# Kernel optimization log

Measured on AMD Instinct MI355X. Metric: run time of the kernel, lower is better.

Reference implementation:

```python
import jax, jax.numpy as jnp
import numpy as np

B, H, W, E = 8, 64, 64, 256  # channels == embedding (required by final Multiply)


def setup_inputs() -> dict:
    key = jax.random.key(0)
    k1, k2, k3 = jax.random.split(key, 3)
    inputs = jax.random.normal(k1, (B, H, W, E), dtype=jnp.float32)
    # Conv2D(embedding, 3, padding='same') params, HWIO layout
    conv_w = jax.random.normal(k2, (3, 3, E, E), dtype=jnp.float32) * (1.0 / np.sqrt(9 * E))
    conv_b = jnp.zeros((E,), dtype=jnp.float32)
    return {"inputs": inputs, "conv_w": conv_w, "conv_b": conv_b}


def reference(inputs, conv_w, conv_b):
    emb = conv_w.shape[-1]
    # conv1: 3x3 same-padded conv, NHWC
    x = jax.lax.conv_general_dilated(
        inputs, conv_w, window_strides=(1, 1), padding="SAME",
        dimension_numbers=("NHWC", "HWIO", "NHWC")) + conv_b
    b, h, w, e = x.shape
    x1 = x.reshape(b, h * w, e)                       # [B, N, E]
    scores = jnp.einsum("bne,bme->bnm", x1, x1)       # [B, N, N]
    attn = jax.nn.softmax(scores, axis=-1) / jnp.sqrt(jnp.asarray(emb, x.dtype))
    out = jnp.einsum("bnm,bme->bne", attn, x1)        # [B, N, E]
    # Original keras uses Reshape((inputs.shape[-2], inputs.shape[-3], -1)): (W, H, E)
    out = out.reshape(b, w, h, e)
    return out * inputs
```

## Files before the change

### kernel.cpp

```cpp
#include <hip/hip_runtime.h>
#include <hip/hip_bf16.h>

typedef __attribute__((ext_vector_type(4))) float f32x4;
typedef __attribute__((ext_vector_type(8))) _Float16 f16x8;
typedef __attribute__((ext_vector_type(16))) float f32x16;
typedef unsigned short u16;

#define NB 8
#define NE 256
#define NN 4096
#define SD 64

__device__ __forceinline__ f32x16 z16() {
  f32x16 v;
#pragma unroll
  for (int i = 0; i < 16; ++i) v[i] = 0.f;
  return v;
}
__device__ __forceinline__ void gload_lds16(const void* g, void* l) {
  __builtin_amdgcn_global_load_lds((const __attribute__((address_space(1))) void*)g,
                                   (__attribute__((address_space(3))) void*)l, 16, 0, 0);
}
__device__ __forceinline__ float fexp2(float x) {
#if __has_builtin(__builtin_amdgcn_exp2f)
  return __builtin_amdgcn_exp2f(x);
#else
  return exp2f(x);
#endif
}

#if __has_builtin(__builtin_amdgcn_permlane32_swap)
typedef int i32x2 __attribute__((ext_vector_type(2)));
__device__ __forceinline__ void plswap(int& a, int& b) {
  i32x2 r = __builtin_amdgcn_permlane32_swap(a, b, false, false);
  a = r[0]; b = r[1];
}
#else
__device__ __forceinline__ void plswap(int& a, int& b) {
  int xa = __shfl_xor(a, 32), xb = __shfl_xor(b, 32);
  int hi = (int)((threadIdx.x & 63) >> 5);
  int na = hi ? xb : a;
  int nb = hi ? b : xa;
  a = na; b = nb;
}
#endif

__global__ __launch_bounds__(256) void k_split(const float* __restrict__ x,
                                               u16* __restrict__ outF, int n4) {
  int i = blockIdx.x * 256 + threadIdx.x;
  if (i >= n4) return;
  float4 v = reinterpret_cast<const float4*>(x)[i];
  ushort4 o;
  o.x = __builtin_bit_cast(u16, (_Float16)v.x);
  o.y = __builtin_bit_cast(u16, (_Float16)v.y);
  o.z = __builtin_bit_cast(u16, (_Float16)v.z);
  o.w = __builtin_bit_cast(u16, (_Float16)v.w);
  reinterpret_cast<ushort4*>(outF)[i] = o;
}

__global__ __launch_bounds__(256) void k_wsplit(const float* __restrict__ w,
                                                u16* __restrict__ wT) {
  int i = blockIdx.x * 256 + threadIdx.x;
  int t = i >> 16;
  int r = i & 65535;
  int ei = r >> 8, eo = r & 255;
  int o = (t << 16) + (eo << 8) + ei;
  wT[o] = __builtin_bit_cast(u16, (_Float16)w[i]);
}

__global__ __launch_bounds__(256, 2) void k_conv(const u16* __restrict__ inF,
                                                 const u16* __restrict__ wT,
                                                 const float* __restrict__ bias,
                                                 u16* __restrict__ x1h) {
  __shared__ u16 Ah[128][72];
  __shared__ u16 BhL[128 * 64];
  int b = blockIdx.x >> 6;
  int rem = blockIdx.x & 63;
  int mt = rem >> 1, et = rem & 1;
  int h0 = mt << 1;
  int tid = threadIdx.x;
  int wid = tid >> 6, lane = tid & 63;
  int wr = wid >> 1, wc = wid & 1;
  int r = lane & 15, g = lane >> 4;
  f32x4 acc[4][4];
#pragma unroll
  for (int i = 0; i < 4; ++i)
#pragma unroll
    for (int j = 0; j < 4; ++j) acc[i][j] = (f32x4){0.f, 0.f, 0.f, 0.f};
  const long ibase = (long)b * NN * NE;
  const int bsw = ((((lane & 7) << 4) ^ (((lane >> 3) & 7) << 4)) >> 1);

#pragma unroll 1
  for (int t = 0; t < 9; ++t) {
    int dy = t / 3 - 1, dx = t % 3 - 1;
#pragma unroll 1
    for (int kc = 0; kc < 4; ++kc) {
      __syncthreads();
      for (int c = tid; c < 1024; c += 256) {
        int pix = c >> 3, c8 = c & 7;
        int ww = pix & 63, hh = h0 + (pix >> 6);
        int sh = hh + dy, sw = ww + dx;
        float4 vh = make_float4(0.f, 0.f, 0.f, 0.f);
        if ((unsigned)sh < 64u && (unsigned)sw < 64u) {
          long off = ibase + ((long)sh * 64 + sw) * NE + kc * 64 + c8 * 8;
          vh = *reinterpret_cast<const float4*>(inF + off);
        }
        *reinterpret_cast<float4*>(&Ah[pix][c8 * 8]) = vh;
      }
#pragma unroll
      for (int i = 0; i < 4; ++i) {
        int c = wid * 4 + i;
        int eo = c * 8 + (lane >> 3);
        const u16* src = wT + ((long)t << 16) + (long)(et * 128 + eo) * 256 + kc * 64 + bsw;
        gload_lds16(src, (char*)BhL + c * 1024);
      }
      __syncthreads();
#pragma unroll
      for (int ks = 0; ks < 2; ++ks) {
        int c8 = ks * 4 + g;
        f16x8 ah[4], bh[4];
#pragma unroll
        for (int mi = 0; mi < 4; ++mi)
          ah[mi] = *reinterpret_cast<const f16x8*>(&Ah[wr * 64 + mi * 16 + r][c8 * 8]);
#pragma unroll
        for (int ni = 0; ni < 4; ++ni) {
          int col = wc * 64 + ni * 16 + r;
          int byteoff = (col << 7) + (((c8 << 4) ^ ((r & 7) << 4)));
          bh[ni] = *reinterpret_cast<const f16x8*>(reinterpret_cast<const char*>(BhL) + byteoff);
        }
#pragma unroll
        for (int mi = 0; mi < 4; ++mi)
#pragma unroll
          for (int ni = 0; ni < 4; ++ni)
            acc[mi][ni] = __builtin_amdgcn_mfma_f32_16x16x32_f16(ah[mi], bh[ni], acc[mi][ni], 0, 0, 0);
      }
    }
  }
#pragma unroll
  for (int mi = 0; mi < 4; ++mi)
#pragma unroll
    for (int ni = 0; ni < 4; ++ni) {
      int eo = et * 128 + wc * 64 + ni * 16 + r;
      float bz = bias[eo];
#pragma unroll
      for (int i = 0; i < 4; ++i) {
        int pix = mt * 128 + wr * 64 + mi * 16 + g * 4 + i;
        float v = acc[mi][ni][i] + bz;
        long o = ibase + (long)pix * NE + eo;
        x1h[o] = __builtin_bit_cast(u16, (_Float16)v);
      }
    }
}

__global__ __launch_bounds__(256) void k_trans(const u16* __restrict__ x1h, u16* __restrict__ x1T) {
  __shared__ u16 T[64][72];
  int bid = blockIdx.x;
  int b = bid >> 8, rem = bid & 255;
  int mt = rem >> 2, et = rem & 3;
  int tid = threadIdx.x;
  for (int c = tid; c < 512; c += 256) {
    int rr = c >> 3, c8 = c & 7;
    *reinterpret_cast<float4*>(&T[rr][c8 * 8]) =
        *reinterpret_cast<const float4*>(x1h + ((long)b * NN + mt * 64 + rr) * NE + et * 64 + c8 * 8);
  }
  __syncthreads();
  for (int c = tid; c < 512; c += 256) {
    int er = c >> 3, m8 = c & 7;
    union { u16 u[8]; float4 v; } p;
#pragma unroll
    for (int j = 0; j < 8; ++j) p.u[j] = T[m8 * 8 + j][er];
    *reinterpret_cast<float4*>(x1T + ((long)b * NE + et * 64 + er) * NN + mt * 64 + m8 * 8) = p.v;
  }
}

__global__ __launch_bounds__(256, 2) void k_flash3(const u16* __restrict__ x1h16,
                                                   const u16* __restrict__ x1T,
                                                   const float* __restrict__ inp,
                                                   float* __restrict__ out) {
  __shared__ char LDS[65536];
  int phys = blockIdx.x;
  int b = phys & 7;
  int qt = phys >> 3;
  int tid = threadIdx.x, wid = tid >> 6, lane = tid & 63;
  int r31 = lane & 31, hi = lane >> 5;
  int eh = wid & 1, qg = wid >> 1;
  const long bN = (long)b << 12;
  const long vtb = (long)b << 20;

  const long qrow = bN + qt * 64 + qg * 32 + r31;
  f16x8 qh[16];
#pragma unroll
  for (int ks = 0; ks < 16; ++ks) {
    qh[ks] = *reinterpret_cast<const f16x8*>(x1h16 + (qrow << 8) + ks * 16 + hi * 8);
#pragma unroll
    for (int j = 0; j < 8; ++j)
      qh[ks][j] = (_Float16)((float)qh[ks][j] * 1.44269504f);
  }

  f32x16 o4[4];
#pragma unroll
  for (int nf = 0; nf < 4; ++nf) o4[nf] = z16();
  float mrow = -1.0e30f, lrow = 0.f;

  const u16* kS[4];
  const u16* vS[4];
  int off[4];
#pragma unroll
  for (int i = 0; i < 4; ++i) {
    int c = wid * 4 + i;
    off[i] = c << 10;
    int kr = c * 2 + (lane >> 5);
    int kcolb = ((lane & 31) << 4) ^ ((kr & 15) << 4);
    kS[i] = x1h16 + ((bN + kr) << 8) + (kcolb >> 1);
    int rp = c * 16 + (lane >> 2);
    int e = rp ^ ((rp >> 2) & 1);
    int vcolb = ((lane & 3) << 4) ^ ((e & 3) << 4);
    vS[i] = x1T + vtb + ((long)e << 12) + (vcolb >> 1);
  }

#pragma unroll
  for (int i = 0; i < 4; ++i) { gload_lds16(kS[i], LDS + off[i]); kS[i] += 8192; }
#pragma unroll
  for (int i = 0; i < 4; ++i) { gload_lds16(vS[i], LDS + 32768 + off[i]); vS[i] += 32; }

#pragma unroll 1
  for (int it = 0; it < 128; ++it) {
    const char* KB = LDS + (it & 1) * 16384;
    const char* VB = LDS + 32768 + (it & 1) * 16384;

    asm volatile("s_waitcnt vmcnt(0)" ::: "memory");
    __builtin_amdgcn_s_barrier();
    __builtin_amdgcn_sched_barrier(0);

    if (it < 127) {
      char* KD = LDS + ((it + 1) & 1) * 16384;
      char* VD = LDS + 32768 + ((it + 1) & 1) * 16384;
#pragma unroll
      for (int i = 0; i < 4; ++i) { gload_lds16(kS[i], KD + off[i]); kS[i] += 8192; }
#pragma unroll
      for (int i = 0; i < 4; ++i) { gload_lds16(vS[i], VD + off[i]); vS[i] += 32; }
    }

    f32x16 stA = z16(), stB = z16();
    int swzk = (r31 & 15) << 4;
    int krow = r31 << 9;
    __builtin_amdgcn_s_setprio(1);
#pragma unroll
    for (int ks = 0; ks < 8; ++ks) {
      int cbyA = ((2 * ks) * 32 + hi * 16) ^ swzk;
      int cbyB = ((2 * ks + 1) * 32 + hi * 16) ^ swzk;
      f16x8 kA = *reinterpret_cast<const f16x8*>(KB + krow + cbyA);
      f16x8 kB = *reinterpret_cast<const f16x8*>(KB + krow + cbyB);
      stA = __builtin_amdgcn_mfma_f32_32x32x16_f16(kA, qh[2 * ks], stA, 0, 0, 0);
      stB = __builtin_amdgcn_mfma_f32_32x32x16_f16(kB, qh[2 * ks + 1], stB, 0, 0, 0);
    }
    __builtin_amdgcn_s_setprio(0);
    f32x16 st;
#pragma unroll
    for (int m = 0; m < 16; ++m) st[m] = stA[m] + stB[m];

    float t8[8];
#pragma unroll
    for (int m = 0; m < 8; ++m) t8[m] = fmaxf(st[m], st[m + 8]);
    float t4a = fmaxf(t8[0], t8[4]), t4b = fmaxf(t8[1], t8[5]);
    float t4c = fmaxf(t8[2], t8[6]), t4d = fmaxf(t8[3], t8[7]);
    float tmax = fmaxf(fmaxf(t4a, t4b), fmaxf(t4c, t4d));
    tmax = fmaxf(tmax, __shfl_xor(tmax, 32));
    if (!__all(tmax <= mrow + 11.54f)) {
      float mnew = fmaxf(mrow, tmax);
      float alpha = fexp2(mrow - mnew);
      lrow *= alpha;
      float ar[16];
#pragma unroll
      for (int m = 0; m < 16; ++m) ar[m] = __shfl(alpha, (m & 3) + 8 * (m >> 2) + 4 * hi);
#pragma unroll
      for (int nf = 0; nf < 4; ++nf)
#pragma unroll
        for (int m = 0; m < 16; ++m) o4[nf][m] *= ar[m];
      mrow = mnew;
    }
#pragma unroll
    for (int m = 0; m < 16; ++m) st[m] = fexp2(st[m] - mrow);
    float s8[8];
#pragma unroll
    for (int m = 0; m < 8; ++m) s8[m] = st[m] + st[m + 8];
    float s4a = s8[0] + s8[4], s4b = s8[1] + s8[5], s4c = s8[2] + s8[6], s4d = s8[3] + s8[7];
    float psum = (s4a + s4b) + (s4c + s4d);
    psum += __shfl_xor(psum, 32);
    lrow += psum;

    int Wd[8];
#pragma unroll
    for (int m = 0; m < 8; ++m) {
      unsigned l0 = __builtin_bit_cast(u16, (_Float16)st[2 * m]);
      unsigned h0 = __builtin_bit_cast(u16, (_Float16)st[2 * m + 1]);
      Wd[m] = (int)(l0 | (h0 << 16));
    }
    plswap(Wd[0], Wd[2]); plswap(Wd[1], Wd[3]);
    plswap(Wd[4], Wd[6]); plswap(Wd[5], Wd[7]);
    union PU { int w[4]; f16x8 v; };
    PU pa[2];
#pragma unroll
    for (int c = 0; c < 2; ++c) {
      pa[c].w[0] = Wd[c * 4 + 0]; pa[c].w[1] = Wd[c * 4 + 1];
      pa[c].w[2] = Wd[c * 4 + 2]; pa[c].w[3] = Wd[c * 4 + 3];
    }

    __builtin_amdgcn_s_setprio(1);
#pragma unroll
    for (int nf = 0; nf < 4; ++nf) {
      int e = eh * 128 + nf * 32 + r31;
      const char* vrow = VB + ((e << 6) ^ ((e & 4) << 4));
      int swzv = (e & 3) << 4;
#pragma unroll
      for (int c = 0; c < 2; ++c) {
        f16x8 v = *reinterpret_cast<const f16x8*>(vrow + ((c * 32 + hi * 16) ^ swzv));
        o4[nf] = __builtin_amdgcn_mfma_f32_32x32x16_f16(pa[c].v, v, o4[nf], 0, 0, 0);
      }
    }
    __builtin_amdgcn_s_setprio(0);
  }

  float linv = 1.0f / (16.0f * lrow);
  float lr[16];
#pragma unroll
  for (int m = 0; m < 16; ++m) lr[m] = __shfl(linv, (m & 3) + 8 * (m >> 2) + 4 * hi);
  const long ob = (bN + qt * 64 + qg * 32) << 8;
#pragma unroll
  for (int nf = 0; nf < 4; ++nf)
#pragma unroll
    for (int m = 0; m < 16; ++m) {
      int qr = (m & 3) + 8 * (m >> 2) + 4 * hi;
      long off2 = ob + ((long)qr << 8) + eh * 128 + nf * 32 + r31;
      out[off2] = o4[nf][m] * lr[m] * inp[off2];
    }
}

extern "C" void kernel_launch(void* const* d_in, const int* in_sizes, int n_in,
                              void* d_out, int out_size, void* d_ws, size_t ws_size,
                              hipStream_t stream) {
  const float* inp   = (const float*)d_in[0];
  const float* convw = (const float*)d_in[1];
  const float* convb = (const float*)d_in[2];
  float* out = (float*)d_out;
  char* ws = (char*)d_ws;

  u16* x1h = (u16*)(ws);
  u16* x1T = (u16*)(ws + 16777216L);
  u16* inF = (u16*)(ws + 33554432L);
  u16* wT  = (u16*)(ws + 50331648L);

  k_split<<<8192, 256, 0, stream>>>(inp, inF, 2097152);
  k_wsplit<<<2304, 256, 0, stream>>>(convw, wT);
  k_conv<<<512, 256, 0, stream>>>(inF, wT, convb, x1h);
  k_trans<<<2048, 256, 0, stream>>>(x1h, x1T);
  k_flash3<<<512, 256, 0, stream>>>(x1h, x1T, inp, out);
}
```

Baseline: 344.0 us.

## Load conv input halo once per channel chunk and double-buffer weight tiles

The conv kernel now loads a 4x66 halo tile of the input into shared memory once per 64-channel chunk, using direct global-to-LDS loads with XOR swizzling and zeroing of out-of-bounds slots. All 9 filter taps then read shifted windows of that tile, so the input is no longer reloaded for every tap. Weight tiles are double-buffered so the next tap's weights load while the current one computes. The two fp16 conversion kernels are merged into one launch. The cost is more shared memory per block, which may reduce occupancy, and extra address bookkeeping.

```diff
diff --git a/kernel.cpp b/kernel.cpp
--- a/kernel.cpp
+++ b/kernel.cpp
@@ -45,35 +45,35 @@
 }
 #endif
 
-__global__ __launch_bounds__(256) void k_split(const float* __restrict__ x,
-                                               u16* __restrict__ outF, int n4) {
-  int i = blockIdx.x * 256 + threadIdx.x;
-  if (i >= n4) return;
-  float4 v = reinterpret_cast<const float4*>(x)[i];
-  ushort4 o;
-  o.x = __builtin_bit_cast(u16, (_Float16)v.x);
-  o.y = __builtin_bit_cast(u16, (_Float16)v.y);
-  o.z = __builtin_bit_cast(u16, (_Float16)v.z);
-  o.w = __builtin_bit_cast(u16, (_Float16)v.w);
-  reinterpret_cast<ushort4*>(outF)[i] = o;
-}
-
-__global__ __launch_bounds__(256) void k_wsplit(const float* __restrict__ w,
-                                                u16* __restrict__ wT) {
-  int i = blockIdx.x * 256 + threadIdx.x;
-  int t = i >> 16;
-  int r = i & 65535;
-  int ei = r >> 8, eo = r & 255;
-  int o = (t << 16) + (eo << 8) + ei;
-  wT[o] = __builtin_bit_cast(u16, (_Float16)w[i]);
+__global__ __launch_bounds__(256) void k_prep(const float* __restrict__ x, u16* __restrict__ outF,
+                                              const float* __restrict__ w, u16* __restrict__ wT) {
+  int bid = blockIdx.x;
+  int tid = threadIdx.x;
+  if (bid < 8192) {
+    int i = bid * 256 + tid;
+    float4 v = reinterpret_cast<const float4*>(x)[i];
+    ushort4 o;
+    o.x = __builtin_bit_cast(u16, (_Float16)v.x);
+    o.y = __builtin_bit_cast(u16, (_Float16)v.y);
+    o.z = __builtin_bit_cast(u16, (_Float16)v.z);
+    o.w = __builtin_bit_cast(u16, (_Float16)v.w);
+    reinterpret_cast<ushort4*>(outF)[i] = o;
+  } else {
+    int i = (bid - 8192) * 256 + tid;
+    int t = i >> 16;
+    int r = i & 65535;
+    int ei = r >> 8, eo = r & 255;
+    int o = (t << 16) + (eo << 8) + ei;
+    wT[o] = __builtin_bit_cast(u16, (_Float16)w[i]);
+  }
 }
 
 __global__ __launch_bounds__(256, 2) void k_conv(const u16* __restrict__ inF,
                                                  const u16* __restrict__ wT,
                                                  const float* __restrict__ bias,
                                                  u16* __restrict__ x1h) {
-  __shared__ u16 Ah[128][72];
-  __shared__ u16 BhL[128 * 64];
+  __shared__ u16 Ahalo[264 * 64];
+  __shared__ u16 BhL[2][128 * 64];
   int b = blockIdx.x >> 6;
   int rem = blockIdx.x & 63;
   int mt = rem >> 1, et = rem & 1;
@@ -88,45 +88,89 @@
 #pragma unroll
     for (int j = 0; j < 4; ++j) acc[i][j] = (f32x4){0.f, 0.f, 0.f, 0.f};
   const long ibase = (long)b * NN * NE;
+
   const int bsw = ((((lane & 7) << 4) ^ (((lane >> 3) & 7) << 4)) >> 1);
+  long bSrc[4];
+#pragma unroll
+  for (int i = 0; i < 4; ++i) {
+    int c = wid * 4 + i;
+    int eo = c * 8 + (lane >> 3);
+    bSrc[i] = (long)(et * 128 + eo) * 256 + bsw;
+  }
+  int aSlot[9], aHalo[9];
+  const u16* aSrc[9];
+#pragma unroll
+  for (int j = 0; j < 9; ++j) {
+    int c = wid + 4 * j;
+    int slot = c * 8 + (lane >> 3);
+    int hr = slot >= 198 ? 3 : (slot >= 132 ? 2 : (slot >= 66 ? 1 : 0));
+    int hc = slot - hr * 66;
+    int ir = h0 - 1 + hr, ic = hc - 1;
+    aHalo[j] = ((unsigned)ir >= 64u) | ((unsigned)ic >= 64u);
+    int irc = min(max(ir, 0), 63), icc = min(max(ic, 0), 63);
+    int c8s = (lane & 7) ^ (slot & 7);
+    aSlot[j] = slot;
+    aSrc[j] = inF + ibase + ((long)(irc * 64 + icc) << 8) + c8s * 8;
+  }
+
+#pragma unroll
+  for (int i = 0; i < 4; ++i)
+    gload_lds16(wT + bSrc[i], (char*)BhL[0] + (wid * 4 + i) * 1024);
 
 #pragma unroll 1
-  for (int t = 0; t < 9; ++t) {
-    int dy = t / 3 - 1, dx = t % 3 - 1;
+  for (int kc = 0; kc < 4; ++kc) {
+    __builtin_amdgcn_s_barrier();
+#pragma unroll
+    for (int j = 0; j < 9; ++j) {
+      int c = wid + 4 * j;
+      if (c < 33)
+        gload_lds16(aSrc[j] + kc * 64, (char*)Ahalo + c * 1024);
+    }
+    asm volatile("s_waitcnt vmcnt(0)" ::: "memory");
+#pragma unroll
+    for (int j = 0; j < 9; ++j) {
+      int c = wid + 4 * j;
+      if (c < 33 && aHalo[j])
+        *reinterpret_cast<float4*>((char*)Ahalo + c * 1024 + (lane << 4)) =
+            make_float4(0.f, 0.f, 0.f, 0.f);
+    }
+    asm volatile("s_waitcnt lgkmcnt(0)" ::: "memory");
+    __builtin_amdgcn_s_barrier();
+
 #pragma unroll 1
-    for (int kc = 0; kc < 4; ++kc) {
-      __syncthreads();
-      for (int c = tid; c < 1024; c += 256) {
-        int pix = c >> 3, c8 = c & 7;
-        int ww = pix & 63, hh = h0 + (pix >> 6);
-        int sh = hh + dy, sw = ww + dx;
-        float4 vh = make_float4(0.f, 0.f, 0.f, 0.f);
-        if ((unsigned)sh < 64u && (unsigned)sw < 64u) {
-          long off = ibase + ((long)sh * 64 + sw) * NE + kc * 64 + c8 * 8;
-          vh = *reinterpret_cast<const float4*>(inF + off);
-        }
-        *reinterpret_cast<float4*>(&Ah[pix][c8 * 8]) = vh;
+    for (int t = 0; t < 9; ++t) {
+      int gidx = kc * 9 + t;
+      if (t > 0) {
+        asm volatile("s_waitcnt vmcnt(0)" ::: "memory");
+        __builtin_amdgcn_s_barrier();
       }
-#pragma unroll
-      for (int i = 0; i < 4; ++i) {
-        int c = wid * 4 + i;
-        int eo = c * 8 + (lane >> 3);
-        const u16* src = wT + ((long)t << 16) + (long)(et * 128 + eo) * 256 + kc * 64 + bsw;
-        gload_lds16(src, (char*)BhL + c * 1024);
+      if (gidx < 35) {
+        int nt = t + 1 == 9 ? 0 : t + 1;
+        int nkc = t + 1 == 9 ? kc + 1 : kc;
+        long tkoff = ((long)nt << 16) + nkc * 64;
+        char* dstB = (char*)BhL[(gidx + 1) & 1];
+#pragma unroll
+        for (int i = 0; i < 4; ++i)
+          gload_lds16(wT + tkoff + bSrc[i], dstB + (wid * 4 + i) * 1024);
       }
-      __syncthreads();
+      const u16* BB = BhL[gidx & 1];
+      int dy = t / 3 - 1, dx = t % 3 - 1;
+      int abase = (wr + 1 + dy) * 66 + 1 + dx;
 #pragma unroll
       for (int ks = 0; ks < 2; ++ks) {
         int c8 = ks * 4 + g;
         f16x8 ah[4], bh[4];
 #pragma unroll
-        for (int mi = 0; mi < 4; ++mi)
-          ah[mi] = *reinterpret_cast<const f16x8*>(&Ah[wr * 64 + mi * 16 + r][c8 * 8]);
+        for (int mi = 0; mi < 4; ++mi) {
+          int slot = abase + mi * 16 + r;
+          int abyte = (slot << 7) + ((c8 << 4) ^ ((slot & 7) << 4));
+          ah[mi] = *reinterpret_cast<const f16x8*>(reinterpret_cast<const char*>(Ahalo) + abyte);
+        }
 #pragma unroll
         for (int ni = 0; ni < 4; ++ni) {
           int col = wc * 64 + ni * 16 + r;
-          int byteoff = (col << 7) + (((c8 << 4) ^ ((r & 7) << 4)));
-          bh[ni] = *reinterpret_cast<const f16x8*>(reinterpret_cast<const char*>(BhL) + byteoff);
+          int bbyte = (col << 7) + ((c8 << 4) ^ ((r & 7) << 4));
+          bh[ni] = *reinterpret_cast<const f16x8*>(reinterpret_cast<const char*>(BB) + bbyte);
         }
 #pragma unroll
         for (int mi = 0; mi < 4; ++mi)
@@ -350,8 +394,7 @@
   u16* inF = (u16*)(ws + 33554432L);
   u16* wT  = (u16*)(ws + 50331648L);
 
-  k_split<<<8192, 256, 0, stream>>>(inp, inF, 2097152);
-  k_wsplit<<<2304, 256, 0, stream>>>(convw, wT);
+  k_prep<<<10496, 256, 0, stream>>>(inp, inF, convw, wT);
   k_conv<<<512, 256, 0, stream>>>(inF, wT, convb, x1h);
   k_trans<<<2048, 256, 0, stream>>>(x1h, x1T);
   k_flash3<<<512, 256, 0, stream>>>(x1h, x1T, inp, out);
```

After: 306.8 us. 10.8% less time.
